# Kernel optimization log

Hardware: AMD Instinct MI355X
Metric: run time of the kernel (lower is better)

Reference implementation:

```python
import jax, jax.numpy as jnp
import numpy as np

N, F_IN, HID, HEADS, NC, E, NG = 50000, 128, 64, 4, 8, 800000, 512


def setup_inputs() -> dict:
    key = jax.random.key(0)
    ks = jax.random.split(key, 16)
    x = jax.random.normal(ks[0], (N, F_IN), dtype=jnp.float32)
    # edges with src != dst so every node's incoming set is exactly {neighbors, self-loop}
    dst = jax.random.randint(ks[1], (E,), 0, N, dtype=jnp.int64)
    off = jax.random.randint(ks[2], (E,), 1, N, dtype=jnp.int64)
    src = (dst + off) % N
    edge_index = jnp.stack([src, dst])
    batch = jnp.sort(jax.random.randint(ks[3], (N,), 0, NG, dtype=jnp.int64))
    g = 1.0 / np.sqrt(F_IN)
    W1 = jax.random.uniform(ks[4], (F_IN, HEADS * HID), jnp.float32, -g, g)
    att_src1 = jax.random.normal(ks[5], (HEADS, HID), jnp.float32) * 0.1
    att_dst1 = jax.random.normal(ks[6], (HEADS, HID), jnp.float32) * 0.1
    b1 = jnp.zeros((HEADS * HID,), jnp.float32)
    g2 = 1.0 / np.sqrt(HEADS * HID)
    W2 = jax.random.uniform(ks[7], (HEADS * HID, HID), jnp.float32, -g2, g2)
    att_src2 = jax.random.normal(ks[8], (1, HID), jnp.float32) * 0.1
    att_dst2 = jax.random.normal(ks[9], (1, HID), jnp.float32) * 0.1
    b2 = jnp.zeros((HID,), jnp.float32)
    g3 = 1.0 / np.sqrt(HID)
    lin_w = jax.random.uniform(ks[10], (HID, NC), jnp.float32, -g3, g3)
    lin_b = jnp.zeros((NC,), jnp.float32)
    return dict(x=x, edge_index=edge_index, batch=batch, W1=W1, att_src1=att_src1,
                att_dst1=att_dst1, b1=b1, W2=W2, att_src2=att_src2, att_dst2=att_dst2,
                b2=b2, lin_w=lin_w, lin_b=lin_b)


def gat_layer(x, src, dst, W, att_s, att_d, bias, heads, out_ch):
    # PyG GATConv: h = x @ W, e_ij = LeakyReLU(a_s.h_j + a_d.h_i), softmax over dst groups
    h = (x @ W).reshape(-1, heads, out_ch)                    # [N,H,C]
    a_s = jnp.einsum('nhc,hc->nh', h, att_s)                  # [N,H]
    a_d = jnp.einsum('nhc,hc->nh', h, att_d)
    e = jax.nn.leaky_relu(a_s[src] + a_d[dst], 0.2)           # [Ef,H]
    m = jax.ops.segment_max(e, dst, num_segments=N)           # stable segment softmax
    ex = jnp.exp(e - m[dst])
    s = jax.ops.segment_sum(ex, dst, num_segments=N)
    alpha = ex / (s[dst] + 1e-16)                             # [Ef,H]
    msg = h[src] * alpha[:, :, None]                          # [Ef,H,C]
    out = jax.ops.segment_sum(msg, dst, num_segments=N)       # [N,H,C]
    return out.reshape(-1, heads * out_ch) + bias, alpha


def reference(x, edge_index, batch, W1, att_src1, att_dst1, b1,
              W2, att_src2, att_dst2, b2, lin_w, lin_b):
    loops = jnp.arange(N, dtype=edge_index.dtype)
    src = jnp.concatenate([edge_index[0], loops])             # add self-loops (PyG default)
    dst = jnp.concatenate([edge_index[1], loops])
    h, alpha1 = gat_layer(x, src, dst, W1, att_src1, att_dst1, b1, HEADS, HID)
    h = jax.nn.relu(h)
    # conv2 on edge_index_1 (already has self-loops; PyG remove+add is a no-op here)
    h, alpha2 = gat_layer(h, src, dst, W2, att_src2, att_dst2, b2, 1, HID)
    h = jax.nn.relu(h)
    sums = jax.ops.segment_sum(h, batch, num_segments=NG)     # global_mean_pool
    cnt = jax.ops.segment_sum(jnp.ones((N,), h.dtype), batch, num_segments=NG)
    pooled = sums / jnp.maximum(cnt, 1.0)[:, None]
    # dropout is identity in eval mode
    return pooled @ lin_w + lin_b
```

## Files before the change

### kernel.cpp

```cpp
#include <hip/hip_runtime.h>

#define F_IN 128
#define HID 64
#define HEADS 4
#define NC 8

typedef __bf16 bf16_t;
typedef bf16_t bf16x8 __attribute__((ext_vector_type(8)));
typedef float f32x4 __attribute__((ext_vector_type(4)));
typedef float f32x2 __attribute__((ext_vector_type(2)));

union BF8 { bf16x8 v; ushort u[8]; };


__device__ __forceinline__ ushort f2bf(float f) {
    uint u = __float_as_uint(f);
    return (ushort)((u + 0x7fffu + ((u >> 16) & 1u)) >> 16);
}
__device__ __forceinline__ float bf2f(ushort h) {
    return __uint_as_float(((uint)h) << 16);
}
__device__ __forceinline__ float edgew(float e) {
    e = (e > 0.f) ? e : 0.2f * e;
    return __expf(e);
}
__device__ __forceinline__ f32x2 unpk(uint u) {
    f32x2 r;
    r.x = __uint_as_float(u << 16);
    r.y = __uint_as_float(u & 0xffff0000u);
    return r;
}

__global__ void k_setup(const float* __restrict__ W1, const float* __restrict__ W2,
                        ushort* __restrict__ w1hi, ushort* __restrict__ w2hi,
                        int* __restrict__ deg, int N, int* __restrict__ counts, int NG) {
    int i = blockIdx.x * blockDim.x + threadIdx.x;
    if (i < N) deg[i] = 1;
    if (i < NG) counts[i] = 0;
    if (i < 128 * 256) {
        int k = i >> 8, n = i & 255;
        int cy = n >> 7, ct = (n >> 4) & 7, c = n & 15, kc = k >> 5, ls = (k >> 3) & 3, j = k & 7;
        size_t off = ((((size_t)cy * 8 + ct) * 4 + kc) * 64 + (ls * 16 + c)) * 8 + j;
        w1hi[off] = f2bf(W1[i]);
    }
    if (i < 256 * 64) {
        int k = i >> 6, n = i & 63;
        int ct = n >> 4, c = n & 15, kc = k >> 5, ls = (k >> 3) & 3, j = k & 7;
        size_t off = (((size_t)ct * 8 + kc) * 64 + (ls * 16 + c)) * 8 + j;
        w2hi[off] = f2bf(W2[i]);
    }
}

__global__ void k_count(const int* __restrict__ ei, int E, int* __restrict__ deg,
                        const int* __restrict__ batch, int N, int* __restrict__ counts) {
    int i = blockIdx.x * blockDim.x + threadIdx.x;
    if (i < E) atomicAdd(&deg[ei[E + i]], 1);
    if (i < N) atomicAdd(&counts[batch[i]], 1);
}

__global__ __launch_bounds__(1024) void k_scan_part(const int* __restrict__ v,
                                                    int* __restrict__ excl,
                                                    int* __restrict__ bsum, int n) {
    __shared__ int buf[1024];
    int tid = threadIdx.x;
    int i = blockIdx.x * 1024 + tid;
    int val = (i < n) ? v[i] : 0;
    buf[tid] = val;
    __syncthreads();
    for (int off = 1; off < 1024; off <<= 1) {
        int t = (tid >= off) ? buf[tid - off] : 0;
        __syncthreads();
        buf[tid] += t;
        __syncthreads();
    }
    if (i < n) excl[i] = buf[tid] - val;
    if (tid == 1023) bsum[blockIdx.x] = buf[1023];
}

__global__ __launch_bounds__(1024) void k_scan_small2(const int* __restrict__ bsum,
                                                      int* __restrict__ boff, int nb,
                                                      int* __restrict__ total_out,
                                                      const int* __restrict__ counts,
                                                      int* __restrict__ gstart, int ng) {
    __shared__ int buf[1024];
    int tid = threadIdx.x;
    const int* src = (blockIdx.x == 0) ? bsum : counts;
    int cnt = (blockIdx.x == 0) ? nb : ng;
    int val = (tid < cnt) ? src[tid] : 0;
    buf[tid] = val;
    __syncthreads();
    for (int off = 1; off < 1024; off <<= 1) {
        int t = (tid >= off) ? buf[tid - off] : 0;
        __syncthreads();
        buf[tid] += t;
        __syncthreads();
    }
    if (blockIdx.x == 0) {
        if (tid < cnt) boff[tid] = buf[tid] - val;
        if (tid == 1023) total_out[0] = buf[1023];
    } else {
        if (tid < cnt) gstart[tid] = buf[tid] - val;
        if (tid == 1023) gstart[ng] = buf[1023];
    }
}

__global__ void k_scan_add_self(int* __restrict__ rowstart, const int* __restrict__ boff,
                                int* __restrict__ cursor, int* __restrict__ csr, int n) {
    int i = blockIdx.x * blockDim.x + threadIdx.x;
    if (i < n) {
        int rs = rowstart[i] + boff[i >> 10];
        rowstart[i] = rs;
        csr[rs] = i;
        cursor[i] = 1;
    }
}

__global__ void k_scatter(const int* __restrict__ ei, int E, const int* __restrict__ rowstart,
                          int* __restrict__ cursor, int* __restrict__ csr) {
    int e = blockIdx.x * blockDim.x + threadIdx.x;
    if (e < E) {
        int d = ei[E + e], s = ei[e];
        int pos = atomicAdd(&cursor[d], 1);
        csr[rowstart[d] + pos] = s;
    }
}

__global__ __launch_bounds__(256) void k_gemm1(const float* __restrict__ x,
                                               const ushort* __restrict__ w1hi,
                                               const float* __restrict__ atts,
                                               const float* __restrict__ attd,
                                               ushort* __restrict__ h1b,
                                               float* __restrict__ as1, float* __restrict__ ad1,
                                               int N) {
    __shared__ __align__(16) ushort lhi[16384];
    int tid = threadIdx.x;
    int cy = blockIdx.y;
    {
        float4* dh = (float4*)lhi; const float4* sh = (const float4*)(w1hi + (size_t)cy * 16384);
        #pragma unroll
        for (int i = 0; i < 8; i++) dh[tid + i * 256] = sh[tid + i * 256];
    }
    __syncthreads();
    int w = tid >> 6, l = tid & 63;
    int lc = l & 15, lk = l >> 4;
    int rbase = blockIdx.x * 256 + w * 64;

    f32x4 acc[4][8];
    #pragma unroll
    for (int mt = 0; mt < 4; mt++)
        #pragma unroll
        for (int ct = 0; ct < 8; ct++) acc[mt][ct] = (f32x4){0.f, 0.f, 0.f, 0.f};

    #pragma unroll
    for (int kc = 0; kc < 4; kc++) {
        BF8 ahi[4];
        #pragma unroll
        for (int mt = 0; mt < 4; mt++) {
            int row = rbase + mt * 16 + lc;
            float4 v0 = {0.f, 0.f, 0.f, 0.f}, v1 = v0;
            if (row < N) {
                const float* xp = x + (size_t)row * F_IN + kc * 32 + lk * 8;
                v0 = *(const float4*)xp; v1 = *(const float4*)(xp + 4);
            }
            float vals[8] = {v0.x, v0.y, v0.z, v0.w, v1.x, v1.y, v1.z, v1.w};
            #pragma unroll
            for (int j = 0; j < 8; j++) ahi[mt].u[j] = f2bf(vals[j]);
        }
        #pragma unroll
        for (int ct = 0; ct < 8; ct++) {
            int boff = ((ct * 4 + kc) * 64 + l) * 8;
            bf16x8 bhi = *(const bf16x8*)(lhi + boff);
            #pragma unroll
            for (int mt = 0; mt < 4; mt++) {
                acc[mt][ct] = __builtin_amdgcn_mfma_f32_16x16x32_bf16(ahi[mt].v, bhi, acc[mt][ct], 0, 0, 0);
            }
        }
    }
    #pragma unroll
    for (int mt = 0; mt < 4; mt++) {
        int rowb = rbase + mt * 16 + lk * 4;
        #pragma unroll
        for (int ct = 0; ct < 8; ct++) {
            int col = cy * 128 + ct * 16 + lc;
            #pragma unroll
            for (int r = 0; r < 4; r++) {
                int row = rowb + r;
                if (row < N) h1b[(size_t)row * 256 + col] = f2bf(acc[mt][ct][r]);
            }
        }
        #pragma unroll
        for (int hh = 0; hh < 2; hh++) {
            float s[4] = {0.f, 0.f, 0.f, 0.f}, d[4] = {0.f, 0.f, 0.f, 0.f};
            #pragma unroll
            for (int cq = 0; cq < 4; cq++) {
                int ct = hh * 4 + cq;
                int col = cy * 128 + ct * 16 + lc;
                float av = atts[col], dv = attd[col];
                #pragma unroll
                for (int r = 0; r < 4; r++) { s[r] += acc[mt][ct][r] * av; d[r] += acc[mt][ct][r] * dv; }
            }
            #pragma unroll
            for (int r = 0; r < 4; r++) {
                #pragma unroll
                for (int off = 1; off < 16; off <<= 1) {
                    s[r] += __shfl_xor(s[r], off);
                    d[r] += __shfl_xor(d[r], off);
                }
            }
            if (lc == 0) {
                int head = cy * 2 + hh;
                #pragma unroll
                for (int r = 0; r < 4; r++) {
                    int row = rowb + r;
                    if (row < N) { as1[row * 4 + head] = s[r]; ad1[row * 4 + head] = d[r]; }
                }
            }
        }
    }
}

__global__ __launch_bounds__(256) void k_fagg1(const ushort* __restrict__ h1b,
                                               const float* __restrict__ as1,
                                               const float* __restrict__ ad1,
                                               const int* __restrict__ rowstart,
                                               const int* __restrict__ csr,
                                               const float* __restrict__ b1,
                                               ushort* __restrict__ out1b, int N) {
    __shared__ float lw[4][256];
    __shared__ int   lsrc[4][64];
    int wid = threadIdx.x >> 6, lane = threadIdx.x & 63;
    int n = blockIdx.x * 4 + wid;
    if (n >= N) return;
    int beg = rowstart[n], end = rowstart[n + 1];
    float4 adv = *(const float4*)(ad1 + (size_t)n * 4);
    int lh = lane & 31, half = lane >> 5;
    int c0 = lh * 8;
    int head = lh >> 3;
    float s0 = 0.f, s1 = 0.f, s2 = 0.f, s3 = 0.f;
    f32x2 a2[4];
    #pragma unroll
    for (int i = 0; i < 4; i++) a2[i] = (f32x2){0.f, 0.f};

    for (int jc = beg; jc < end; jc += 64) {
        int j = jc + lane;
        float4 wv = {0.f, 0.f, 0.f, 0.f};
        int src = 0;
        if (j < end) {
            src = csr[j];
            float4 av = *(const float4*)(as1 + (size_t)src * 4);
            wv.x = edgew(av.x + adv.x); wv.y = edgew(av.y + adv.y);
            wv.z = edgew(av.z + adv.z); wv.w = edgew(av.w + adv.w);
            s0 += wv.x; s1 += wv.y; s2 += wv.z; s3 += wv.w;
        }
        *(float4*)&lw[wid][lane * 4] = wv;
        lsrc[wid][lane] = src;
        int cnt = min(64, end - jc);
        int pairs = (cnt + 1) >> 1;
        for (int t = 0; t < pairs; t += 8) {
            #pragma unroll
            for (int u = 0; u < 8; u++) {
                int tt = t + u;
                if (tt < pairs) {
                    int e = 2 * tt + half;
                    int sr = lsrc[wid][e];
                    float wgt = lw[wid][e * 4 + head];
                    uint4 hv = *(const uint4*)(h1b + (size_t)sr * 256 + c0);
                    f32x2 ws = {wgt, wgt};
                    a2[0] += ws * unpk(hv.x);
                    a2[1] += ws * unpk(hv.y);
                    a2[2] += ws * unpk(hv.z);
                    a2[3] += ws * unpk(hv.w);
                }
            }
        }
    }
    #pragma unroll
    for (int i = 0; i < 4; i++) {
        a2[i].x += __shfl_xor(a2[i].x, 32);
        a2[i].y += __shfl_xor(a2[i].y, 32);
    }
    #pragma unroll
    for (int off = 1; off < 64; off <<= 1) {
        s0 += __shfl_xor(s0, off); s1 += __shfl_xor(s1, off);
        s2 += __shfl_xor(s2, off); s3 += __shfl_xor(s3, off);
    }
    float sv = (head == 0) ? s0 : (head == 1) ? s1 : (head == 2) ? s2 : s3;
    float inv = 1.f / sv;
    if (half == 0) {
        const float4* bv = (const float4*)(b1 + c0);
        float4 bA = bv[0], bB = bv[1];
        float o0 = fmaxf(a2[0].x * inv + bA.x, 0.f), o1 = fmaxf(a2[0].y * inv + bA.y, 0.f);
        float o2 = fmaxf(a2[1].x * inv + bA.z, 0.f), o3 = fmaxf(a2[1].y * inv + bA.w, 0.f);
        float o4 = fmaxf(a2[2].x * inv + bB.x, 0.f), o5 = fmaxf(a2[2].y * inv + bB.y, 0.f);
        float o6 = fmaxf(a2[3].x * inv + bB.z, 0.f), o7 = fmaxf(a2[3].y * inv + bB.w, 0.f);
        uint4 ov;
        ov.x = (uint)f2bf(o0) | ((uint)f2bf(o1) << 16);
        ov.y = (uint)f2bf(o2) | ((uint)f2bf(o3) << 16);
        ov.z = (uint)f2bf(o4) | ((uint)f2bf(o5) << 16);
        ov.w = (uint)f2bf(o6) | ((uint)f2bf(o7) << 16);
        *(uint4*)(out1b + (size_t)n * 256 + c0) = ov;
    }
}

__global__ __launch_bounds__(256) void k_gemm2(const ushort* __restrict__ xin,
                                               const ushort* __restrict__ w2hi,
                                               const float* __restrict__ atts,
                                               const float* __restrict__ attd,
                                               ushort* __restrict__ h2b,
                                               float* __restrict__ as2, float* __restrict__ ad2,
                                               int N) {
    __shared__ __align__(16) ushort lhi[16384];
    int tid = threadIdx.x;
    {
        float4* dh = (float4*)lhi; const float4* sh = (const float4*)w2hi;
        #pragma unroll
        for (int i = 0; i < 8; i++) dh[tid + i * 256] = sh[tid + i * 256];
    }
    __syncthreads();
    int w = tid >> 6, l = tid & 63;
    int lc = l & 15, lk = l >> 4;
    int rbase = blockIdx.x * 256 + w * 64;

    f32x4 acc[4][4];
    #pragma unroll
    for (int mt = 0; mt < 4; mt++)
        #pragma unroll
        for (int ct = 0; ct < 4; ct++) acc[mt][ct] = (f32x4){0.f, 0.f, 0.f, 0.f};

    #pragma unroll
    for (int kc = 0; kc < 8; kc++) {
        BF8 a[4];
        #pragma unroll
        for (int mt = 0; mt < 4; mt++) {
            int row = rbase + mt * 16 + lc;
            if (row < N) {
                a[mt].v = *(const bf16x8*)(xin + (size_t)row * 256 + kc * 32 + lk * 8);
            } else {
                #pragma unroll
                for (int j = 0; j < 8; j++) a[mt].u[j] = 0;
            }
        }
        #pragma unroll
        for (int ct = 0; ct < 4; ct++) {
            bf16x8 bhi = *(const bf16x8*)(lhi + ((ct * 8 + kc) * 64 + l) * 8);
            #pragma unroll
            for (int mt = 0; mt < 4; mt++) {
                acc[mt][ct] = __builtin_amdgcn_mfma_f32_16x16x32_bf16(a[mt].v, bhi, acc[mt][ct], 0, 0, 0);
            }
        }
    }
    #pragma unroll
    for (int mt = 0; mt < 4; mt++) {
        int rowb = rbase + mt * 16 + lk * 4;
        #pragma unroll
        for (int ct = 0; ct < 4; ct++) {
            int col = ct * 16 + lc;
            #pragma unroll
            for (int r = 0; r < 4; r++) {
                int row = rowb + r;
                if (row < N) h2b[(size_t)row * 64 + col] = f2bf(acc[mt][ct][r]);
            }
        }
        float s[4] = {0.f, 0.f, 0.f, 0.f}, d[4] = {0.f, 0.f, 0.f, 0.f};
        #pragma unroll
        for (int ct = 0; ct < 4; ct++) {
            int col = ct * 16 + lc;
            float av = atts[col], dv = attd[col];
            #pragma unroll
            for (int r = 0; r < 4; r++) { s[r] += acc[mt][ct][r] * av; d[r] += acc[mt][ct][r] * dv; }
        }
        #pragma unroll
        for (int r = 0; r < 4; r++) {
            #pragma unroll
            for (int off = 1; off < 16; off <<= 1) {
                s[r] += __shfl_xor(s[r], off);
                d[r] += __shfl_xor(d[r], off);
            }
        }
        if (lc == 0) {
            #pragma unroll
            for (int r = 0; r < 4; r++) {
                int row = rowb + r;
                if (row < N) { as2[row] = s[r]; ad2[row] = d[r]; }
            }
        }
    }
}

__global__ __launch_bounds__(256) void k_fagg2(const ushort* __restrict__ h2b,
                                               const float* __restrict__ as2,
                                               const float* __restrict__ ad2,
                                               const int* __restrict__ rowstart,
                                               const int* __restrict__ csr,
                                               const float* __restrict__ b2,
                                               float* __restrict__ out2, int N) {
    __shared__ float lw[4][64];
    __shared__ int   lsrc[4][64];
    int wid = threadIdx.x >> 6, lane = threadIdx.x & 63;
    int n = blockIdx.x * 4 + wid;
    if (n >= N) return;
    int beg = rowstart[n], end = rowstart[n + 1];
    float adv = ad2[n];
    int g = lane >> 3, li = lane & 7;
    int c0 = li * 8;
    float ss = 0.f;
    f32x2 a2[4];
    #pragma unroll
    for (int i = 0; i < 4; i++) a2[i] = (f32x2){0.f, 0.f};

    for (int jc = beg; jc < end; jc += 64) {
        int j = jc + lane;
        float wgt = 0.f;
        int src = 0;
        if (j < end) {
            src = csr[j];
            wgt = edgew(as2[src] + adv);
            ss += wgt;
        }
        lw[wid][lane] = wgt;
        lsrc[wid][lane] = src;
        int cnt = min(64, end - jc);
        int groups = (cnt + 7) >> 3;
        for (int t = 0; t < groups; t += 2) {
            #pragma unroll
            for (int u = 0; u < 2; u++) {
                int tt = t + u;
                if (tt < groups) {
                    int e = tt * 8 + g;
                    int sr = lsrc[wid][e];
                    float wv = lw[wid][e];
                    uint4 hv = *(const uint4*)(h2b + (size_t)sr * 64 + c0);
                    f32x2 ws = {wv, wv};
                    a2[0] += ws * unpk(hv.x);
                    a2[1] += ws * unpk(hv.y);
                    a2[2] += ws * unpk(hv.z);
                    a2[3] += ws * unpk(hv.w);
                }
            }
        }
    }
    #pragma unroll
    for (int i = 0; i < 4; i++) {
        a2[i].x += __shfl_xor(a2[i].x, 8);
        a2[i].x += __shfl_xor(a2[i].x, 16);
        a2[i].x += __shfl_xor(a2[i].x, 32);
        a2[i].y += __shfl_xor(a2[i].y, 8);
        a2[i].y += __shfl_xor(a2[i].y, 16);
        a2[i].y += __shfl_xor(a2[i].y, 32);
    }
    #pragma unroll
    for (int off = 1; off < 64; off <<= 1) ss += __shfl_xor(ss, off);
    float inv = 1.f / ss;
    if (g == 0) {
        const float4* bv = (const float4*)(b2 + c0);
        float4 bA = bv[0], bB = bv[1];
        float4 oA, oB;
        oA.x = fmaxf(a2[0].x * inv + bA.x, 0.f); oA.y = fmaxf(a2[0].y * inv + bA.y, 0.f);
        oA.z = fmaxf(a2[1].x * inv + bA.z, 0.f); oA.w = fmaxf(a2[1].y * inv + bA.w, 0.f);
        oB.x = fmaxf(a2[2].x * inv + bB.x, 0.f); oB.y = fmaxf(a2[2].y * inv + bB.y, 0.f);
        oB.z = fmaxf(a2[3].x * inv + bB.z, 0.f); oB.w = fmaxf(a2[3].y * inv + bB.w, 0.f);
        float* op = out2 + (size_t)n * 64 + c0;
        *(float4*)op = oA;
        *(float4*)(op + 4) = oB;
    }
}


__global__ __launch_bounds__(64) void k_pool(const float* __restrict__ out2,
                                             const int* __restrict__ gstart,
                                             const float* __restrict__ lin_w,
                                             const float* __restrict__ lin_b,
                                             float* __restrict__ out, int NG) {
    __shared__ float mean[64];
    int g = blockIdx.x;
    int lane = threadIdx.x;
    int beg = gstart[g], end = gstart[g + 1];
    float s = 0.f;
    for (int n = beg; n < end; n++) s += out2[(size_t)n * 64 + lane];
    float cnt = (float)(end - beg);
    mean[lane] = s / fmaxf(cnt, 1.f);
    __syncthreads();
    if (lane < NC) {
        float acc = lin_b[lane];
        #pragma unroll
        for (int c = 0; c < 64; c++) acc += mean[c] * lin_w[c * NC + lane];
        out[g * NC + lane] = acc;
    }
}


extern "C" void kernel_launch(void* const* d_in, const int* in_sizes, int n_in,
                              void* d_out, int out_size, void* d_ws, size_t ws_size,
                              hipStream_t stream) {
    const float* x      = (const float*)d_in[0];
    const int*   ei     = (const int*)d_in[1];
    const int*   batch  = (const int*)d_in[2];
    const float* W1     = (const float*)d_in[3];
    const float* att_s1 = (const float*)d_in[4];
    const float* att_d1 = (const float*)d_in[5];
    const float* b1     = (const float*)d_in[6];
    const float* W2     = (const float*)d_in[7];
    const float* att_s2 = (const float*)d_in[8];
    const float* att_d2 = (const float*)d_in[9];
    const float* b2     = (const float*)d_in[10];
    const float* lin_w  = (const float*)d_in[11];
    const float* lin_b  = (const float*)d_in[12];
    float* out = (float*)d_out;

    const int N  = in_sizes[0] / F_IN;
    const int E  = in_sizes[1] / 2;
    const int NG = out_size / NC;
    const int NE = E + N;
    const int NB = (N + 1023) / 1024;

    char* p = (char*)d_ws;
    auto alloc = [&](size_t bytes) { char* r = p; p += (bytes + 255) & ~(size_t)255; return r; };
    ushort* h1b     = (ushort*)alloc(sizeof(ushort) * (size_t)N * 256);
    ushort* out1b   = (ushort*)alloc(sizeof(ushort) * (size_t)N * 256);
    ushort* h2b     = (ushort*)alloc(sizeof(ushort) * (size_t)N * 64);
    float*  out2    = (float*)alloc(sizeof(float) * (size_t)N * 64);
    float*  as1     = (float*)alloc(sizeof(float) * (size_t)N * 4);
    float*  ad1     = (float*)alloc(sizeof(float) * (size_t)N * 4);
    float*  as2     = (float*)alloc(sizeof(float) * (size_t)N);
    float*  ad2     = (float*)alloc(sizeof(float) * (size_t)N);
    int*    rowstart= (int*)alloc(sizeof(int) * (size_t)(N + 1));
    int*    itmp    = (int*)alloc(sizeof(int) * (size_t)N);
    int*    csr     = (int*)alloc(sizeof(int) * (size_t)NE);
    int*    counts  = (int*)alloc(sizeof(int) * (size_t)NG);
    int*    gstart  = (int*)alloc(sizeof(int) * (size_t)(NG + 1));
    int*    bsum    = (int*)alloc(sizeof(int) * 1024);
    int*    boff    = (int*)alloc(sizeof(int) * 1024);
    ushort* w1hi    = (ushort*)alloc(sizeof(ushort) * 32768);
    ushort* w2hi    = (ushort*)alloc(sizeof(ushort) * 16384);

    int bs = 256;
    k_setup<<<(N + bs - 1) / bs, bs, 0, stream>>>(W1, W2, w1hi, w2hi, itmp, N, counts, NG);
    k_count<<<(E + bs - 1) / bs, bs, 0, stream>>>(ei, E, itmp, batch, N, counts);
    k_scan_part<<<NB, 1024, 0, stream>>>(itmp, rowstart, bsum, N);
    k_scan_small2<<<2, 1024, 0, stream>>>(bsum, boff, NB, rowstart + N, counts, gstart, NG);
    k_scan_add_self<<<(N + 1023) / 1024, 1024, 0, stream>>>(rowstart, boff, itmp, csr, N);
    k_scatter<<<(E + bs - 1) / bs, bs, 0, stream>>>(ei, E, rowstart, itmp, csr);

    k_gemm1<<<dim3((N + 255) / 256, 2), 256, 0, stream>>>(x, w1hi, att_s1, att_d1, h1b, as1, ad1, N);
    k_fagg1<<<(N + 3) / 4, 256, 0, stream>>>(h1b, as1, ad1, rowstart, csr, b1, out1b, N);

    k_gemm2<<<(N + 255) / 256, 256, 0, stream>>>(out1b, w2hi, att_s2, att_d2, h2b, as2, ad2, N);
    k_fagg2<<<(N + 3) / 4, 256, 0, stream>>>(h2b, as2, ad2, rowstart, csr, b2, out2, N);

    k_pool<<<NG, 64, 0, stream>>>(out2, gstart, lin_w, lin_b, out, NG);
}
```

Baseline: 301.1 us.

## Fuse CSR graph-build kernels into one cooperative kernel with grid syncs

Replaces the six preprocessing kernels (weight conversion, degree counting, two-level scan, self-loop insert, edge scatter) with one cooperative kernel. Phases are separated by grid-wide syncs and use grid-stride loops, and the scan block size drops from 1024 to 256 threads. This removes several kernel launches and the gaps between them. In exchange it adds grid barrier cost and runs the work on a fixed 512-block grid.

```diff
diff --git a/kernel.cpp b/kernel.cpp
--- a/kernel.cpp
+++ b/kernel.cpp
@@ -1,4 +1,7 @@
 #include <hip/hip_runtime.h>
+#include <hip/hip_cooperative_groups.h>
+
+namespace cg = cooperative_groups;
 
 #define F_IN 128
 #define HID 64
@@ -31,96 +34,114 @@
     return r;
 }
 
-__global__ void k_setup(const float* __restrict__ W1, const float* __restrict__ W2,
-                        ushort* __restrict__ w1hi, ushort* __restrict__ w2hi,
-                        int* __restrict__ deg, int N, int* __restrict__ counts, int NG) {
-    int i = blockIdx.x * blockDim.x + threadIdx.x;
-    if (i < N) deg[i] = 1;
-    if (i < NG) counts[i] = 0;
-    if (i < 128 * 256) {
+__global__ __launch_bounds__(256) void k_build(
+    const float* __restrict__ W1, const float* __restrict__ W2,
+    ushort* __restrict__ w1hi, ushort* __restrict__ w2hi,
+    const int* __restrict__ ei, const int* __restrict__ batch,
+    int E, int N, int NG,
+    int* __restrict__ deg,
+    int* __restrict__ counts,
+    int* __restrict__ rowstart,
+    int* __restrict__ bsum, int* __restrict__ boff,
+    int* __restrict__ gstart,
+    int* __restrict__ csr) {
+    cg::grid_group grid = cg::this_grid();
+    __shared__ int sbuf[256];
+    __shared__ int scarry;
+    int tid = threadIdx.x;
+    int gid = blockIdx.x * 256 + tid;
+    int GS = gridDim.x * 256;
+
+    for (int i = gid; i < N; i += GS) deg[i] = 1;
+    for (int i = gid; i < NG; i += GS) counts[i] = 0;
+    for (int i = gid; i < 128 * 256; i += GS) {
         int k = i >> 8, n = i & 255;
         int cy = n >> 7, ct = (n >> 4) & 7, c = n & 15, kc = k >> 5, ls = (k >> 3) & 3, j = k & 7;
         size_t off = ((((size_t)cy * 8 + ct) * 4 + kc) * 64 + (ls * 16 + c)) * 8 + j;
         w1hi[off] = f2bf(W1[i]);
     }
-    if (i < 256 * 64) {
+    for (int i = gid; i < 256 * 64; i += GS) {
         int k = i >> 6, n = i & 63;
         int ct = n >> 4, c = n & 15, kc = k >> 5, ls = (k >> 3) & 3, j = k & 7;
         size_t off = (((size_t)ct * 8 + kc) * 64 + (ls * 16 + c)) * 8 + j;
         w2hi[off] = f2bf(W2[i]);
     }
-}
-
-__global__ void k_count(const int* __restrict__ ei, int E, int* __restrict__ deg,
-                        const int* __restrict__ batch, int N, int* __restrict__ counts) {
-    int i = blockIdx.x * blockDim.x + threadIdx.x;
-    if (i < E) atomicAdd(&deg[ei[E + i]], 1);
-    if (i < N) atomicAdd(&counts[batch[i]], 1);
-}
-
-__global__ __launch_bounds__(1024) void k_scan_part(const int* __restrict__ v,
-                                                    int* __restrict__ excl,
-                                                    int* __restrict__ bsum, int n) {
-    __shared__ int buf[1024];
-    int tid = threadIdx.x;
-    int i = blockIdx.x * 1024 + tid;
-    int val = (i < n) ? v[i] : 0;
-    buf[tid] = val;
-    __syncthreads();
-    for (int off = 1; off < 1024; off <<= 1) {
-        int t = (tid >= off) ? buf[tid - off] : 0;
+    grid.sync();
+
+    for (int i = gid; i < E; i += GS) atomicAdd(&deg[ei[E + i]], 1);
+    for (int i = gid; i < N; i += GS) atomicAdd(&counts[batch[i]], 1);
+    grid.sync();
+
+    int nb = (N + 255) >> 8;
+    if ((int)blockIdx.x < nb) {
+        int i = blockIdx.x * 256 + tid;
+        int val = (i < N) ? deg[i] : 0;
+        sbuf[tid] = val;
         __syncthreads();
-        buf[tid] += t;
+        for (int off = 1; off < 256; off <<= 1) {
+            int t = (tid >= off) ? sbuf[tid - off] : 0;
+            __syncthreads();
+            sbuf[tid] += t;
+            __syncthreads();
+        }
+        if (i < N) rowstart[i] = sbuf[tid] - val;
+        if (tid == 255) bsum[blockIdx.x] = sbuf[255];
+    }
+    grid.sync();
+
+    if (blockIdx.x == 0) {
+        int val = (tid < nb) ? bsum[tid] : 0;
+        sbuf[tid] = val;
         __syncthreads();
-    }
-    if (i < n) excl[i] = buf[tid] - val;
-    if (tid == 1023) bsum[blockIdx.x] = buf[1023];
-}
-
-__global__ __launch_bounds__(1024) void k_scan_small2(const int* __restrict__ bsum,
-                                                      int* __restrict__ boff, int nb,
-                                                      int* __restrict__ total_out,
-                                                      const int* __restrict__ counts,
-                                                      int* __restrict__ gstart, int ng) {
-    __shared__ int buf[1024];
-    int tid = threadIdx.x;
-    const int* src = (blockIdx.x == 0) ? bsum : counts;
-    int cnt = (blockIdx.x == 0) ? nb : ng;
-    int val = (tid < cnt) ? src[tid] : 0;
-    buf[tid] = val;
-    __syncthreads();
-    for (int off = 1; off < 1024; off <<= 1) {
-        int t = (tid >= off) ? buf[tid - off] : 0;
+        for (int off = 1; off < 256; off <<= 1) {
+            int t = (tid >= off) ? sbuf[tid - off] : 0;
+            __syncthreads();
+            sbuf[tid] += t;
+            __syncthreads();
+        }
+        if (tid < nb) boff[tid] = sbuf[tid] - val;
+        if (tid == 255) rowstart[N] = sbuf[255];
+    } else if (blockIdx.x == 1) {
+        int v0 = (tid < NG) ? counts[tid] : 0;
+        sbuf[tid] = v0;
         __syncthreads();
-        buf[tid] += t;
+        for (int off = 1; off < 256; off <<= 1) {
+            int t = (tid >= off) ? sbuf[tid - off] : 0;
+            __syncthreads();
+            sbuf[tid] += t;
+            __syncthreads();
+        }
+        if (tid < NG) gstart[tid] = sbuf[tid] - v0;
+        if (tid == 255) scarry = sbuf[255];
         __syncthreads();
-    }
-    if (blockIdx.x == 0) {
-        if (tid < cnt) boff[tid] = buf[tid] - val;
-        if (tid == 1023) total_out[0] = buf[1023];
-    } else {
-        if (tid < cnt) gstart[tid] = buf[tid] - val;
-        if (tid == 1023) gstart[ng] = buf[1023];
-    }
-}
-
-__global__ void k_scan_add_self(int* __restrict__ rowstart, const int* __restrict__ boff,
-                                int* __restrict__ cursor, int* __restrict__ csr, int n) {
-    int i = blockIdx.x * blockDim.x + threadIdx.x;
-    if (i < n) {
-        int rs = rowstart[i] + boff[i >> 10];
+        int carry = scarry;
+        int i2 = 256 + tid;
+        int v1 = (i2 < NG) ? counts[i2] : 0;
+        __syncthreads();
+        sbuf[tid] = v1;
+        __syncthreads();
+        for (int off = 1; off < 256; off <<= 1) {
+            int t = (tid >= off) ? sbuf[tid - off] : 0;
+            __syncthreads();
+            sbuf[tid] += t;
+            __syncthreads();
+        }
+        if (i2 < NG) gstart[i2] = carry + sbuf[tid] - v1;
+        if (tid == 255) gstart[NG] = carry + sbuf[255];
+    }
+    grid.sync();
+
+    for (int i = gid; i < N; i += GS) {
+        int rs = rowstart[i] + boff[i >> 8];
         rowstart[i] = rs;
         csr[rs] = i;
-        cursor[i] = 1;
-    }
-}
-
-__global__ void k_scatter(const int* __restrict__ ei, int E, const int* __restrict__ rowstart,
-                          int* __restrict__ cursor, int* __restrict__ csr) {
-    int e = blockIdx.x * blockDim.x + threadIdx.x;
-    if (e < E) {
+        deg[i] = 1;
+    }
+    grid.sync();
+
+    for (int e = gid; e < E; e += GS) {
         int d = ei[E + e], s = ei[e];
-        int pos = atomicAdd(&cursor[d], 1);
+        int pos = atomicAdd(&deg[d], 1);
         csr[rowstart[d] + pos] = s;
     }
 }
@@ -507,11 +528,10 @@
     const float* lin_b  = (const float*)d_in[12];
     float* out = (float*)d_out;
 
-    const int N  = in_sizes[0] / F_IN;
-    const int E  = in_sizes[1] / 2;
-    const int NG = out_size / NC;
+    int N  = in_sizes[0] / F_IN;
+    int E  = in_sizes[1] / 2;
+    int NG = out_size / NC;
     const int NE = E + N;
-    const int NB = (N + 1023) / 1024;
 
     char* p = (char*)d_ws;
     auto alloc = [&](size_t bytes) { char* r = p; p += (bytes + 255) & ~(size_t)255; return r; };
@@ -533,13 +553,13 @@
     ushort* w1hi    = (ushort*)alloc(sizeof(ushort) * 32768);
     ushort* w2hi    = (ushort*)alloc(sizeof(ushort) * 16384);
 
-    int bs = 256;
-    k_setup<<<(N + bs - 1) / bs, bs, 0, stream>>>(W1, W2, w1hi, w2hi, itmp, N, counts, NG);
-    k_count<<<(E + bs - 1) / bs, bs, 0, stream>>>(ei, E, itmp, batch, N, counts);
-    k_scan_part<<<NB, 1024, 0, stream>>>(itmp, rowstart, bsum, N);
-    k_scan_small2<<<2, 1024, 0, stream>>>(bsum, boff, NB, rowstart + N, counts, gstart, NG);
-    k_scan_add_self<<<(N + 1023) / 1024, 1024, 0, stream>>>(rowstart, boff, itmp, csr, N);
-    k_scatter<<<(E + bs - 1) / bs, bs, 0, stream>>>(ei, E, rowstart, itmp, csr);
+    void* kargs[] = {
+        (void*)&W1, (void*)&W2, (void*)&w1hi, (void*)&w2hi,
+        (void*)&ei, (void*)&batch, (void*)&E, (void*)&N, (void*)&NG,
+        (void*)&itmp, (void*)&counts, (void*)&rowstart,
+        (void*)&bsum, (void*)&boff, (void*)&gstart, (void*)&csr
+    };
+    hipLaunchCooperativeKernel((void*)k_build, dim3(512), dim3(256), kargs, 0, stream);
 
     k_gemm1<<<dim3((N + 255) / 256, 2), 256, 0, stream>>>(x, w1hi, att_s1, att_d1, h1b, as1, ad1, N);
     k_fagg1<<<(N + 3) / 4, 256, 0, stream>>>(h1b, as1, ad1, rowstart, csr, b1, out1b, N);
```

After: 533.1 us. 77.0% more time.
